# Optimization experiments

Hardware: AMD Instinct MI355X
Metric: run time of the kernel (lower is better)

## Reference

```python
import jax, jax.numpy as jnp
import numpy as np

N = 20000      # nodes
E = 160000     # edges
F_IN = 64      # node_feature_dim
HID = 256      # hidden_dim (= per-head out_channels, concat=False)
HEADS = 4
OUT = 2
BN_EPS = 1e-5


def setup_inputs() -> dict:
    key = jax.random.key(0)
    ks = jax.random.split(key, 24)
    s = 0.02

    def w(k, shape):
        return jax.random.normal(k, shape, jnp.float32) * s

    return {
        "node_feature": jax.random.normal(ks[0], (N, F_IN), jnp.float32),
        "edge_index": jax.random.randint(ks[1], (2, E), 0, N, jnp.int32),
        # layer 1 (in=F_IN)
        "wq1": w(ks[2], (F_IN, HEADS * HID)), "bq1": w(ks[3], (HEADS * HID,)),
        "wk1": w(ks[4], (F_IN, HEADS * HID)), "bk1": w(ks[5], (HEADS * HID,)),
        "wv1": w(ks[6], (F_IN, HEADS * HID)), "bv1": w(ks[7], (HEADS * HID,)),
        "ws1": w(ks[8], (F_IN, HID)),        "bs1": w(ks[9], (HID,)),
        # layer 2 (in=HID)
        "wq2": w(ks[10], (HID, HEADS * HID)), "bq2": w(ks[11], (HEADS * HID,)),
        "wk2": w(ks[12], (HID, HEADS * HID)), "bk2": w(ks[13], (HEADS * HID,)),
        "wv2": w(ks[14], (HID, HEADS * HID)), "bv2": w(ks[15], (HEADS * HID,)),
        "ws2": w(ks[16], (HID, HID)),         "bs2": w(ks[17], (HID,)),
        # batch norm affine
        "bn_gamma": jnp.ones((HID,), jnp.float32) + w(ks[18], (HID,)),
        "bn_beta": w(ks[19], (HID,)),
        # final linear
        "lin_w": w(ks[20], (HID, OUT)), "lin_b": w(ks[21], (OUT,)),
    }


def _transformer_conv(x, src, dst, wq, bq, wk, bk, wv, bv, ws, bs):
    """PyG TransformerConv, heads=HEADS, concat=False (mean over heads), root_weight."""
    n = x.shape[0]
    q = (x @ wq + bq).reshape(n, HEADS, HID)   # [N,H,C]
    k = (x @ wk + bk).reshape(n, HEADS, HID)
    v = (x @ wv + bv).reshape(n, HEADS, HID)
    # per-edge attention logits: q_i . k_j / sqrt(C)   (message j->i, i = dst)
    alpha = jnp.einsum('ehc,ehc->eh', q[dst], k[src]) / jnp.sqrt(jnp.float32(HID))  # [E,H]
    # scatter-softmax over incoming edges of each target node
    m = jax.ops.segment_max(alpha, dst, num_segments=n)
    m = jnp.where(jnp.isfinite(m), m, 0.0)  # nodes with no in-edges
    ex = jnp.exp(alpha - m[dst])
    denom = jax.ops.segment_sum(ex, dst, num_segments=n)
    a = ex / (denom[dst] + 1e-16)                          # [E,H]
    out = jax.ops.segment_sum(v[src] * a[..., None], dst, num_segments=n)  # [N,H,C]
    return out.mean(axis=1) + x @ ws + bs                  # concat=False -> head mean; + skip


def reference(node_feature, edge_index,
              wq1, bq1, wk1, bk1, wv1, bv1, ws1, bs1,
              wq2, bq2, wk2, bk2, wv2, bv2, ws2, bs2,
              bn_gamma, bn_beta, lin_w, lin_b):
    src, dst = edge_index[0], edge_index[1]
    x = _transformer_conv(node_feature, src, dst, wq1, bq1, wk1, bk1, wv1, bv1, ws1, bs1)
    x = _transformer_conv(x, src, dst, wq2, bq2, wk2, bk2, wv2, bv2, ws2, bs2)
    # BatchNorm1d (training mode: batch statistics, biased variance)
    mu = x.mean(axis=0)
    var = jnp.mean(jnp.square(x - mu), axis=0)
    x = bn_gamma * (x - mu) / jnp.sqrt(var + BN_EPS) + bn_beta
    rsu_embedding = x[0:1]                     # [1, HID]
    logits = jax.nn.relu(x @ lin_w + lin_b)    # [N, OUT]
    action_prob = jax.nn.softmax(logits, axis=1)
    return (action_prob, rsu_embedding)
```

## Files before the change

### kernel.cpp

```cpp
#include <hip/hip_runtime.h>
#include <hip/hip_bf16.h>
#include <math.h>

#define DI __device__ __forceinline__

constexpr int NN   = 20000;
constexpr int NE   = 160000;
constexpr int FIN  = 64;
constexpr int HIDC = 256;
constexpr int NH   = 4;
constexpr int NOUT = 3328;
constexpr int CAPD = 128;

typedef __attribute__((ext_vector_type(8))) short short8;
typedef __attribute__((ext_vector_type(4))) float f32x4;
typedef __attribute__((ext_vector_type(2))) float f32x2;

DI float bf2f(unsigned short u) { return __uint_as_float(((unsigned)u) << 16); }

DI void gld16(const void* g, void* l) {
  __builtin_amdgcn_global_load_lds((const __attribute__((address_space(1))) unsigned*)g,
                                   (__attribute__((address_space(3))) unsigned*)l, 16, 0, 0);
}

DI unsigned fp8pack4(float a, float b, float c, float d) {
  int v = __builtin_amdgcn_cvt_pk_fp8_f32(a, b, 0, false);
  v = __builtin_amdgcn_cvt_pk_fp8_f32(c, d, v, true);
  return (unsigned)v;
}

__global__ void k_prep(const float* __restrict__ x, __hip_bfloat16* __restrict__ xb,
                       const int* __restrict__ dst, int* __restrict__ deg) {
  int gid = blockIdx.x * 256 + threadIdx.x;
  if (gid < NN * FIN) xb[gid] = __float2bfloat16(x[gid]);
  if (gid < NE) atomicAdd(&deg[dst[gid]], 1);
}

__global__ void k_scan(const int* __restrict__ deg, int* __restrict__ offs,
                       int* __restrict__ cursor, int n_) {
  __shared__ int part[1024];
  int tid = threadIdx.x;
  const int CH = (n_ + 1023) >> 10;
  int base = tid * CH;
  int s = 0;
  for (int i = 0; i < CH; ++i) { int idx = base + i; if (idx < n_) s += deg[idx]; }
  part[tid] = s;
  __syncthreads();
  for (int off = 1; off < 1024; off <<= 1) {
    int v = (tid >= off) ? part[tid - off] : 0;
    __syncthreads();
    part[tid] += v;
    __syncthreads();
  }
  int run = (tid == 0) ? 0 : part[tid - 1];
  for (int i = 0; i < CH; ++i) {
    int idx = base + i;
    if (idx < n_) { offs[idx] = run; cursor[idx] = run; run += deg[idx]; }
  }
  if (tid == 1023) offs[n_] = run;
}

__global__ void k_scatter(const int* __restrict__ dst, int* __restrict__ cursor,
                          int* __restrict__ eid, int e_) {
  int e = blockIdx.x * blockDim.x + threadIdx.x;
  if (e < e_) {
    int p = atomicAdd(&cursor[dst[e]], 1);
    eid[p] = e;
  }
}

template <int K>
__global__ void k_pack(const float* __restrict__ wq, const float* __restrict__ bq,
                       const float* __restrict__ wk, const float* __restrict__ bk,
                       const float* __restrict__ wv, const float* __restrict__ bv,
                       const float* __restrict__ ws, const float* __restrict__ bs,
                       __hip_bfloat16* __restrict__ Wt, float* __restrict__ biasp) {
  int n = blockIdx.x * 128 + threadIdx.x;
  int k = blockIdx.y;
  const float* w; const float* b; int off; int M;
  if (n < 1024)      { w = wq; b = bq; off = n;        M = 1024; }
  else if (n < 2048) { w = wk; b = bk; off = n - 1024; M = 1024; }
  else if (n < 3072) { w = wv; b = bv; off = n - 2048; M = 1024; }
  else               { w = ws; b = bs; off = n - 3072; M = 256;  }
  Wt[(size_t)n * K + k] = __float2bfloat16(w[(size_t)k * M + off]);
  if (k == 0) biasp[n] = b[off];
}

template <int K>
__global__ __launch_bounds__(64, 2) void k_gemm_pw(
    const __hip_bfloat16* __restrict__ X, const __hip_bfloat16* __restrict__ Wt,
    const float* __restrict__ biasp,
    unsigned char* __restrict__ qb, unsigned char* __restrict__ kb,
    unsigned char* __restrict__ vb, __hip_bfloat16* __restrict__ skipb,
    int nrows, int NCB, int NCH, int TPC, int RT) {
  __shared__ char lds[16384 + 2304];
  const int l = threadIdx.x;

  const int nwg = NCB * NCH;
  const int per = nwg >> 3;
  const int w = (blockIdx.x & 7) * per + (blockIdx.x >> 3);
  const int chunk = w / NCB;
  const int ct = w % NCB;
  const int bn = ct * 64;
  const int t0 = chunk * TPC;
  int t1 = t0 + TPC; if (t1 > RT) t1 = RT;
  constexpr int KT = K / 64;
  constexpr int NS = K / 32;

  const int lm = l & 15, lk = l >> 4;

  short8 bfr[4 * NS];
  {
    const __hip_bfloat16* bp = Wt + (size_t)(bn + lm) * K + lk * 8;
#pragma unroll
    for (int n = 0; n < 4; ++n)
#pragma unroll
      for (int s = 0; s < NS; ++s)
        bfr[n * NS + s] = *(const short8*)(bp + (size_t)n * 16 * K + s * 32);
  }
  float bia[4];
#pragma unroll
  for (int n = 0; n < 4; ++n) bia[n] = biasp[bn + n * 16 + lm];

  unsigned char* dst8 = nullptr; int cb8 = 0;
  if (bn < 1024)      { dst8 = qb; cb8 = bn; }
  else if (bn < 2048) { dst8 = kb; cb8 = bn - 1024; }
  else if (bn < 3072) { dst8 = vb; cb8 = bn - 2048; }

  const int jrow = l >> 3;
  const int cslot = (l & 7) ^ jrow;
  auto STAGE = [&](int buf, int t, int kt) {
    char* db = lds + buf * 8192;
#pragma unroll
    for (int j = 0; j < 8; ++j) {
      int r = t * 64 + j * 8 + jrow;
      if (r >= nrows) r = nrows - 1;
      gld16(X + (size_t)r * K + kt * 64 + cslot * 8, db + j * 1024 + l * 16);
    }
  };

  int buf = 0;
  STAGE(0, t0, 0);
  for (int t = t0; t < t1; ++t) {
    f32x4 acc[4][4] = {};
#pragma unroll
    for (int kt = 0; kt < KT; ++kt) {
      int nt = t, nk = kt + 1;
      if (nk == KT) { nt = (t + 1 < t1) ? t + 1 : t; nk = 0; }
      STAGE(buf ^ 1, nt, nk);
      asm volatile("s_waitcnt vmcnt(8)" ::: "memory");
      const char* db = lds + buf * 8192;
#pragma unroll
      for (int s2 = 0; s2 < 2; ++s2) {
        short8 a[4];
#pragma unroll
        for (int m = 0; m < 4; ++m) {
          int row = m * 16 + lm;
          a[m] = *(const short8*)(db + row * 128 + (((s2 * 4 + lk) ^ (lm & 7)) * 16));
        }
#pragma unroll
        for (int m = 0; m < 4; ++m)
#pragma unroll
          for (int n = 0; n < 4; ++n)
            acc[m][n] = __builtin_amdgcn_mfma_f32_16x16x32_bf16(
                a[m], bfr[n * NS + kt * 2 + s2], acc[m][n], 0, 0, 0);
      }
      buf ^= 1;
    }

    char* sc = lds + 16384;
    const int tbase = t * 64;
    const int srow = l >> 2, qc = l & 3;
#pragma unroll
    for (int m = 0; m < 4; ++m) {
#pragma unroll
      for (int n = 0; n < 4; ++n)
#pragma unroll
        for (int r = 0; r < 4; ++r)
          *(__hip_bfloat16*)(sc + (lk * 4 + r) * 144 + (n * 16 + lm) * 2) =
              __float2bfloat16(acc[m][n][r] + bia[n]);
      const char* sr = sc + srow * 144 + qc * 32;
      short8 ta = *(const short8*)(sr);
      short8 tb = *(const short8*)(sr + 16);
      int grow = tbase + m * 16 + srow;
      if (grow < nrows) {
        if (dst8 != nullptr) {
          uint4 d;
          d.x = fp8pack4(bf2f((unsigned short)ta[0]), bf2f((unsigned short)ta[1]),
                         bf2f((unsigned short)ta[2]), bf2f((unsigned short)ta[3]));
          d.y = fp8pack4(bf2f((unsigned short)ta[4]), bf2f((unsigned short)ta[5]),
                         bf2f((unsigned short)ta[6]), bf2f((unsigned short)ta[7]));
          d.z = fp8pack4(bf2f((unsigned short)tb[0]), bf2f((unsigned short)tb[1]),
                         bf2f((unsigned short)tb[2]), bf2f((unsigned short)tb[3]));
          d.w = fp8pack4(bf2f((unsigned short)tb[4]), bf2f((unsigned short)tb[5]),
                         bf2f((unsigned short)tb[6]), bf2f((unsigned short)tb[7]));
          *(uint4*)(dst8 + (size_t)grow * 1024 + cb8 + qc * 16) = d;
        } else {
          __hip_bfloat16* sp = skipb + (size_t)grow * HIDC + (bn - 3072) + qc * 16;
          *(short8*)(sp) = ta;
          *(short8*)(sp + 8) = tb;
        }
      }
    }
  }
  asm volatile("s_waitcnt vmcnt(0)" ::: "memory");
}

__global__ __launch_bounds__(256) void k_attn(
    const unsigned char* __restrict__ qb, const unsigned char* __restrict__ kb,
    const unsigned char* __restrict__ vb,
    const int* __restrict__ offs, const int* __restrict__ eid,
    const int* __restrict__ src, const __hip_bfloat16* __restrict__ skipb,
    __hip_bfloat16* __restrict__ outb, float* __restrict__ outf) {
  int n = blockIdx.x;
  int s0 = offs[n], s1 = offs[n + 1];
  int deg = s1 - s0;
  int tid = threadIdx.x;
  if (deg == 0) {
    if (tid < 64) {
      int c = tid * 4;
      ushort4 sv = *(const ushort4*)((const ushort*)skipb + (size_t)n * HIDC + c);
      if (outb != nullptr) *(ushort4*)((ushort*)outb + (size_t)n * HIDC + c) = sv;
      if (outf != nullptr) {
        float* xr = outf + (size_t)n * HIDC + c;
        xr[0] = bf2f(sv.x); xr[1] = bf2f(sv.y); xr[2] = bf2f(sv.z); xr[3] = bf2f(sv.w);
      }
    }
    return;
  }
  __shared__ int ses[CAPD];
  __shared__ float red[NH][HIDC];
  int h = tid >> 6, lane = tid & 63;
  int dc = deg < CAPD ? deg : CAPD;
  for (int i = tid; i < dc; i += 256) ses[i] = src[eid[s0 + i]];
  __syncthreads();

  const int hc = h * HIDC;
  int c = lane * 4;
  unsigned qu = *(const unsigned*)(qb + (size_t)n * 1024 + hc + c);
  f32x2 q01 = __builtin_amdgcn_cvt_pk_f32_fp8(qu, false);
  f32x2 q23 = __builtin_amdgcn_cvt_pk_f32_fp8(qu, true);
  float qx = q01.x, qy = q01.y, qz = q23.x, qw = q23.y;

  float denom = 0.f;
  float4 acc = make_float4(0.f, 0.f, 0.f, 0.f);
  int sc0 = ses[0];
  unsigned ku0 = *(const unsigned*)(kb + (size_t)sc0 * 1024 + hc + c);
  unsigned vu0 = *(const unsigned*)(vb + (size_t)sc0 * 1024 + hc + c);
  for (int i = 0; i < deg; ++i) {
    unsigned ku1 = 0, vu1 = 0;
    if (i + 1 < deg) {
      int s1i = (i + 1 < CAPD) ? ses[i + 1] : src[eid[s0 + i + 1]];
      ku1 = *(const unsigned*)(kb + (size_t)s1i * 1024 + hc + c);
      vu1 = *(const unsigned*)(vb + (size_t)s1i * 1024 + hc + c);
    }
    f32x2 k01 = __builtin_amdgcn_cvt_pk_f32_fp8(ku0, false);
    f32x2 k23 = __builtin_amdgcn_cvt_pk_f32_fp8(ku0, true);
    float p = qx * k01.x + qy * k01.y + qz * k23.x + qw * k23.y;
#pragma unroll
    for (int off = 32; off > 0; off >>= 1) p += __shfl_xor(p, off);
    float wgt = __expf(p * 0.0625f);
    denom += wgt;
    f32x2 v01 = __builtin_amdgcn_cvt_pk_f32_fp8(vu0, false);
    f32x2 v23 = __builtin_amdgcn_cvt_pk_f32_fp8(vu0, true);
    acc.x = fmaf(wgt, v01.x, acc.x);
    acc.y = fmaf(wgt, v01.y, acc.y);
    acc.z = fmaf(wgt, v23.x, acc.z);
    acc.w = fmaf(wgt, v23.y, acc.w);
    ku0 = ku1; vu0 = vu1;
  }
  float dinv = 1.f / (denom + 1e-16f);
  red[h][c + 0] = acc.x * dinv;
  red[h][c + 1] = acc.y * dinv;
  red[h][c + 2] = acc.z * dinv;
  red[h][c + 3] = acc.w * dinv;
  __syncthreads();
  if (tid < 64) {
    int c0 = tid * 4;
    ushort4 sv = *(const ushort4*)((const ushort*)skipb + (size_t)n * HIDC + c0);
    float sk[4] = {bf2f(sv.x), bf2f(sv.y), bf2f(sv.z), bf2f(sv.w)};
#pragma unroll
    for (int j = 0; j < 4; ++j) {
      float m = (red[0][c0 + j] + red[1][c0 + j] + red[2][c0 + j] + red[3][c0 + j]) * 0.25f;
      float val = m + sk[j];
      if (outb != nullptr) ((ushort*)outb)[(size_t)n * HIDC + c0 + j] = (ushort)(__bfloat16_as_ushort(__float2bfloat16(val)));
      if (outf != nullptr) outf[(size_t)n * HIDC + c0 + j] = val;
    }
  }
}

__global__ void k_bnstats(const float* __restrict__ x, float* __restrict__ sums,
                          float* __restrict__ sumsq, int n_) {
  int t = threadIdx.x;
  float s = 0.f, s2 = 0.f;
  for (int r = blockIdx.x; r < n_; r += gridDim.x) {
    float vv = x[(size_t)r * HIDC + t];
    s += vv; s2 += vv * vv;
  }
  atomicAdd(&sums[t], s);
  atomicAdd(&sumsq[t], s2);
}

__global__ __launch_bounds__(256) void k_final(
    const float* __restrict__ x, const float* __restrict__ sums, const float* __restrict__ sumsq,
    const float* __restrict__ gamma, const float* __restrict__ beta,
    const float* __restrict__ lw, const float* __restrict__ lb,
    float* __restrict__ out, int n_) {
  int sub = threadIdx.x >> 6, lane = threadIdx.x & 63;
  int n = blockIdx.x * 4 + sub;
  if (n >= n_) return;
  int c = lane * 4;
  float4 sm  = *(const float4*)(sums + c);
  float4 sq  = *(const float4*)(sumsq + c);
  const float inv_n = 1.f / (float)n_;
  float mu0 = sm.x * inv_n, mu1 = sm.y * inv_n, mu2 = sm.z * inv_n, mu3 = sm.w * inv_n;
  float r0 = 1.f / sqrtf(fmaxf(sq.x * inv_n - mu0 * mu0, 0.f) + 1e-5f);
  float r1 = 1.f / sqrtf(fmaxf(sq.y * inv_n - mu1 * mu1, 0.f) + 1e-5f);
  float r2 = 1.f / sqrtf(fmaxf(sq.z * inv_n - mu2 * mu2, 0.f) + 1e-5f);
  float r3 = 1.f / sqrtf(fmaxf(sq.w * inv_n - mu3 * mu3, 0.f) + 1e-5f);
  const float* xr = x + (size_t)n * HIDC;
  float4 xv = *(const float4*)(xr + c);
  float4 gv = *(const float4*)(gamma + c);
  float4 bv = *(const float4*)(beta + c);
  float y0 = gv.x * (xv.x - mu0) * r0 + bv.x;
  float y1 = gv.y * (xv.y - mu1) * r1 + bv.y;
  float y2 = gv.z * (xv.z - mu2) * r2 + bv.z;
  float y3 = gv.w * (xv.w - mu3) * r3 + bv.w;
  float4 wa = *(const float4*)(lw + (size_t)c * 2);
  float4 wb = *(const float4*)(lw + (size_t)c * 2 + 4);
  float p0 = y0 * wa.x + y1 * wa.z + y2 * wb.x + y3 * wb.z;
  float p1 = y0 * wa.y + y1 * wa.w + y2 * wb.y + y3 * wb.w;
#pragma unroll
  for (int off = 32; off > 0; off >>= 1) {
    p0 += __shfl_xor(p0, off);
    p1 += __shfl_xor(p1, off);
  }
  if (n == 0) *(float4*)(out + (size_t)NN * 2 + c) = make_float4(y0, y1, y2, y3);
  if (lane == 0) {
    float l0 = fmaxf(p0 + lb[0], 0.f);
    float l1 = fmaxf(p1 + lb[1], 0.f);
    float m = fmaxf(l0, l1);
    float e0 = expf(l0 - m), e1 = expf(l1 - m);
    float inv = 1.f / (e0 + e1);
    out[(size_t)n * 2 + 0] = e0 * inv;
    out[(size_t)n * 2 + 1] = e1 * inv;
  }
}

extern "C" void kernel_launch(void* const* d_in, const int* in_sizes, int n_in,
                              void* d_out, int out_size, void* d_ws, size_t ws_size,
                              hipStream_t stream) {
  const float* x0  = (const float*)d_in[0];
  const int*   ei  = (const int*)d_in[1];
  const float* wq1 = (const float*)d_in[2];  const float* bq1 = (const float*)d_in[3];
  const float* wk1 = (const float*)d_in[4];  const float* bk1 = (const float*)d_in[5];
  const float* wv1 = (const float*)d_in[6];  const float* bv1 = (const float*)d_in[7];
  const float* ws1 = (const float*)d_in[8];  const float* bs1 = (const float*)d_in[9];
  const float* wq2 = (const float*)d_in[10]; const float* bq2 = (const float*)d_in[11];
  const float* wk2 = (const float*)d_in[12]; const float* bk2 = (const float*)d_in[13];
  const float* wv2 = (const float*)d_in[14]; const float* bv2 = (const float*)d_in[15];
  const float* ws2 = (const float*)d_in[16]; const float* bs2 = (const float*)d_in[17];
  const float* gam = (const float*)d_in[18]; const float* bet = (const float*)d_in[19];
  const float* lw  = (const float*)d_in[20]; const float* lb  = (const float*)d_in[21];
  const int* srcv = ei;
  const int* dstv = ei + NE;

  char* p = (char*)d_ws;
  auto take = [&](size_t bytes) {
    char* r = p;
    p += (bytes + 255) & ~(size_t)255;
    return r;
  };
  unsigned char* qbuf = (unsigned char*)take((size_t)NN * 1024);
  unsigned char* kbuf = (unsigned char*)take((size_t)NN * 1024);
  unsigned char* vbuf = (unsigned char*)take((size_t)NN * 1024);
  __hip_bfloat16* skipb = (__hip_bfloat16*)take((size_t)NN * HIDC * 2);
  __hip_bfloat16* x0b = (__hip_bfloat16*)take((size_t)NN * FIN * 2);
  __hip_bfloat16* x2b = (__hip_bfloat16*)take((size_t)NN * HIDC * 2);
  __hip_bfloat16* Wt  = (__hip_bfloat16*)take((size_t)NOUT * HIDC * 2);
  float* x3    = (float*)take((size_t)NN * HIDC * 4);
  float* biasp = (float*)take((size_t)NOUT * 4);
  float* bnbuf = (float*)take(2 * HIDC * 4);
  int* deg    = (int*)take((size_t)NN * 4);
  int* offs   = (int*)take((size_t)(NN + 1) * 4);
  int* cursor = (int*)take((size_t)NN * 4);
  int* eidb   = (int*)take((size_t)NE * 4);
  if ((size_t)(p - (char*)d_ws) > ws_size) return;

  float* sums  = bnbuf;
  float* sumsq = bnbuf + HIDC;

  hipMemsetAsync(deg, 0, (size_t)NN * 4, stream);
  hipMemsetAsync(bnbuf, 0, 2 * HIDC * 4, stream);
  k_prep<<<(NN * FIN + 255) / 256, 256, 0, stream>>>(x0, x0b, dstv, deg);
  k_scan<<<1, 1024, 0, stream>>>(deg, offs, cursor, NN);
  k_scatter<<<(NE + 255) / 256, 256, 0, stream>>>(dstv, cursor, eidb, NE);

  const int RT  = (NN + 63) / 64;
  const int NCB = NOUT / 64;
  const int NCH = 40;
  const int TPC = (RT + NCH - 1) / NCH;
  const int GRID = NCB * NCH;
  k_pack<FIN><<<dim3(NOUT / 128, FIN), 128, 0, stream>>>(wq1, bq1, wk1, bk1, wv1, bv1, ws1, bs1, Wt, biasp);
  k_gemm_pw<FIN><<<GRID, 64, 0, stream>>>(x0b, Wt, biasp, qbuf, kbuf, vbuf, skipb, NN, NCB, NCH, TPC, RT);
  k_attn<<<NN, 256, 0, stream>>>(qbuf, kbuf, vbuf, offs, eidb, srcv, skipb, x2b, nullptr);
  k_pack<HIDC><<<dim3(NOUT / 128, HIDC), 128, 0, stream>>>(wq2, bq2, wk2, bk2, wv2, bv2, ws2, bs2, Wt, biasp);
  k_gemm_pw<HIDC><<<GRID, 64, 0, stream>>>(x2b, Wt, biasp, qbuf, kbuf, vbuf, skipb, NN, NCB, NCH, TPC, RT);
  k_attn<<<NN, 256, 0, stream>>>(qbuf, kbuf, vbuf, offs, eidb, srcv, skipb, nullptr, x3);
  k_bnstats<<<256, 256, 0, stream>>>(x3, sums, sumsq, NN);
  k_final<<<(NN + 3) / 4, 256, 0, stream>>>(x3, sums, sumsq, gam, bet, lw, lb, (float*)d_out, NN);
}
```

Before: 362.8 us.

## Store Q/K/V in bf16 and skip in fp32, restructure edge-parallel attention

Q/K/V intermediates move from fp8 to bf16 and the skip branch from bf16 to fp32. That doubles Q/K/V memory traffic but improves accuracy. The attention kernel now processes four edges at once per head, with each lane handling 16 channels and partial sums reduced by shuffles. The in-edge lists are sorted per node so results are deterministic. BatchNorm statistics use a two-stage reduction instead of float atomics, which makes the sums order-independent. Overall this mainly trades bandwidth for precision and determinism, and it adds a sort kernel and an extra reduction launch.

```diff
diff --git a/kernel.cpp b/kernel.cpp
--- a/kernel.cpp
+++ b/kernel.cpp
@@ -14,19 +14,12 @@
 
 typedef __attribute__((ext_vector_type(8))) short short8;
 typedef __attribute__((ext_vector_type(4))) float f32x4;
-typedef __attribute__((ext_vector_type(2))) float f32x2;
 
 DI float bf2f(unsigned short u) { return __uint_as_float(((unsigned)u) << 16); }
 
 DI void gld16(const void* g, void* l) {
   __builtin_amdgcn_global_load_lds((const __attribute__((address_space(1))) unsigned*)g,
                                    (__attribute__((address_space(3))) unsigned*)l, 16, 0, 0);
-}
-
-DI unsigned fp8pack4(float a, float b, float c, float d) {
-  int v = __builtin_amdgcn_cvt_pk_fp8_f32(a, b, 0, false);
-  v = __builtin_amdgcn_cvt_pk_fp8_f32(c, d, v, true);
-  return (unsigned)v;
 }
 
 __global__ void k_prep(const float* __restrict__ x, __hip_bfloat16* __restrict__ xb,
@@ -69,6 +62,18 @@
   }
 }
 
+__global__ void k_sort(const int* __restrict__ offs, int* __restrict__ eid, int n_) {
+  int n = blockIdx.x * 256 + threadIdx.x;
+  if (n >= n_) return;
+  int s0 = offs[n], s1 = offs[n + 1];
+  for (int i = s0 + 1; i < s1; ++i) {
+    int v = eid[i];
+    int j = i - 1;
+    while (j >= s0 && eid[j] > v) { eid[j + 1] = eid[j]; --j; }
+    eid[j + 1] = v;
+  }
+}
+
 template <int K>
 __global__ void k_pack(const float* __restrict__ wq, const float* __restrict__ bq,
                        const float* __restrict__ wk, const float* __restrict__ bk,
@@ -90,8 +95,8 @@
 __global__ __launch_bounds__(64, 2) void k_gemm_pw(
     const __hip_bfloat16* __restrict__ X, const __hip_bfloat16* __restrict__ Wt,
     const float* __restrict__ biasp,
-    unsigned char* __restrict__ qb, unsigned char* __restrict__ kb,
-    unsigned char* __restrict__ vb, __hip_bfloat16* __restrict__ skipb,
+    __hip_bfloat16* __restrict__ qb, __hip_bfloat16* __restrict__ kb,
+    __hip_bfloat16* __restrict__ vb, float* __restrict__ skipf,
     int nrows, int NCB, int NCH, int TPC, int RT) {
   __shared__ char lds[16384 + 2304];
   const int l = threadIdx.x;
@@ -122,10 +127,10 @@
 #pragma unroll
   for (int n = 0; n < 4; ++n) bia[n] = biasp[bn + n * 16 + lm];
 
-  unsigned char* dst8 = nullptr; int cb8 = 0;
-  if (bn < 1024)      { dst8 = qb; cb8 = bn; }
-  else if (bn < 2048) { dst8 = kb; cb8 = bn - 1024; }
-  else if (bn < 3072) { dst8 = vb; cb8 = bn - 2048; }
+  __hip_bfloat16* dst16 = nullptr; int cb16 = 0;
+  if (bn < 1024)      { dst16 = qb; cb16 = bn; }
+  else if (bn < 2048) { dst16 = kb; cb16 = bn - 1024; }
+  else if (bn < 3072) { dst16 = vb; cb16 = bn - 2048; }
 
   const int jrow = l >> 3;
   const int cslot = (l & 7) ^ jrow;
@@ -168,49 +173,49 @@
       buf ^= 1;
     }
 
-    char* sc = lds + 16384;
     const int tbase = t * 64;
-    const int srow = l >> 2, qc = l & 3;
-#pragma unroll
-    for (int m = 0; m < 4; ++m) {
-#pragma unroll
-      for (int n = 0; n < 4; ++n)
-#pragma unroll
-        for (int r = 0; r < 4; ++r)
-          *(__hip_bfloat16*)(sc + (lk * 4 + r) * 144 + (n * 16 + lm) * 2) =
-              __float2bfloat16(acc[m][n][r] + bia[n]);
-      const char* sr = sc + srow * 144 + qc * 32;
-      short8 ta = *(const short8*)(sr);
-      short8 tb = *(const short8*)(sr + 16);
-      int grow = tbase + m * 16 + srow;
-      if (grow < nrows) {
-        if (dst8 != nullptr) {
-          uint4 d;
-          d.x = fp8pack4(bf2f((unsigned short)ta[0]), bf2f((unsigned short)ta[1]),
-                         bf2f((unsigned short)ta[2]), bf2f((unsigned short)ta[3]));
-          d.y = fp8pack4(bf2f((unsigned short)ta[4]), bf2f((unsigned short)ta[5]),
-                         bf2f((unsigned short)ta[6]), bf2f((unsigned short)ta[7]));
-          d.z = fp8pack4(bf2f((unsigned short)tb[0]), bf2f((unsigned short)tb[1]),
-                         bf2f((unsigned short)tb[2]), bf2f((unsigned short)tb[3]));
-          d.w = fp8pack4(bf2f((unsigned short)tb[4]), bf2f((unsigned short)tb[5]),
-                         bf2f((unsigned short)tb[6]), bf2f((unsigned short)tb[7]));
-          *(uint4*)(dst8 + (size_t)grow * 1024 + cb8 + qc * 16) = d;
-        } else {
-          __hip_bfloat16* sp = skipb + (size_t)grow * HIDC + (bn - 3072) + qc * 16;
-          *(short8*)(sp) = ta;
-          *(short8*)(sp + 8) = tb;
+    if (dst16 != nullptr) {
+      char* sc = lds + 16384;
+      const int srow = l >> 2, qc = l & 3;
+#pragma unroll
+      for (int m = 0; m < 4; ++m) {
+#pragma unroll
+        for (int n = 0; n < 4; ++n)
+#pragma unroll
+          for (int r = 0; r < 4; ++r)
+            *(__hip_bfloat16*)(sc + (lk * 4 + r) * 144 + (n * 16 + lm) * 2) =
+                __float2bfloat16(acc[m][n][r] + bia[n]);
+        const char* sr = sc + srow * 144 + qc * 32;
+        short8 ta = *(const short8*)(sr);
+        short8 tb = *(const short8*)(sr + 16);
+        int grow = tbase + m * 16 + srow;
+        if (grow < nrows) {
+          ushort* o = (ushort*)dst16 + (size_t)grow * 1024 + cb16 + qc * 16;
+          *(short8*)o = ta;
+          *(short8*)(o + 8) = tb;
         }
       }
+    } else {
+      const int cb = bn - 3072;
+#pragma unroll
+      for (int m = 0; m < 4; ++m)
+#pragma unroll
+        for (int n = 0; n < 4; ++n)
+#pragma unroll
+          for (int r = 0; r < 4; ++r) {
+            int row = tbase + m * 16 + lk * 4 + r;
+            if (row < nrows) skipf[(size_t)row * HIDC + cb + n * 16 + lm] = acc[m][n][r] + bia[n];
+          }
     }
   }
   asm volatile("s_waitcnt vmcnt(0)" ::: "memory");
 }
 
 __global__ __launch_bounds__(256) void k_attn(
-    const unsigned char* __restrict__ qb, const unsigned char* __restrict__ kb,
-    const unsigned char* __restrict__ vb,
+    const __hip_bfloat16* __restrict__ qb, const __hip_bfloat16* __restrict__ kb,
+    const __hip_bfloat16* __restrict__ vb,
     const int* __restrict__ offs, const int* __restrict__ eid,
-    const int* __restrict__ src, const __hip_bfloat16* __restrict__ skipb,
+    const int* __restrict__ src, const float* __restrict__ skipf,
     __hip_bfloat16* __restrict__ outb, float* __restrict__ outf) {
   int n = blockIdx.x;
   int s0 = offs[n], s1 = offs[n + 1];
@@ -219,86 +224,117 @@
   if (deg == 0) {
     if (tid < 64) {
       int c = tid * 4;
-      ushort4 sv = *(const ushort4*)((const ushort*)skipb + (size_t)n * HIDC + c);
-      if (outb != nullptr) *(ushort4*)((ushort*)outb + (size_t)n * HIDC + c) = sv;
-      if (outf != nullptr) {
-        float* xr = outf + (size_t)n * HIDC + c;
-        xr[0] = bf2f(sv.x); xr[1] = bf2f(sv.y); xr[2] = bf2f(sv.z); xr[3] = bf2f(sv.w);
+      float4 sv = *(const float4*)(skipf + (size_t)n * HIDC + c);
+      if (outb != nullptr) {
+        ushort* ob = (ushort*)outb + (size_t)n * HIDC + c;
+        ob[0] = __bfloat16_as_ushort(__float2bfloat16(sv.x));
+        ob[1] = __bfloat16_as_ushort(__float2bfloat16(sv.y));
+        ob[2] = __bfloat16_as_ushort(__float2bfloat16(sv.z));
+        ob[3] = __bfloat16_as_ushort(__float2bfloat16(sv.w));
       }
+      if (outf != nullptr) *(float4*)(outf + (size_t)n * HIDC + c) = sv;
     }
     return;
   }
   __shared__ int ses[CAPD];
   __shared__ float red[NH][HIDC];
   int h = tid >> 6, lane = tid & 63;
+  int g = lane >> 4, j = lane & 15;
   int dc = deg < CAPD ? deg : CAPD;
   for (int i = tid; i < dc; i += 256) ses[i] = src[eid[s0 + i]];
   __syncthreads();
 
-  const int hc = h * HIDC;
-  int c = lane * 4;
-  unsigned qu = *(const unsigned*)(qb + (size_t)n * 1024 + hc + c);
-  f32x2 q01 = __builtin_amdgcn_cvt_pk_f32_fp8(qu, false);
-  f32x2 q23 = __builtin_amdgcn_cvt_pk_f32_fp8(qu, true);
-  float qx = q01.x, qy = q01.y, qz = q23.x, qw = q23.y;
-
+  float q[16];
+  {
+    const ushort* qr = (const ushort*)qb + (size_t)n * 1024 + h * 256 + j * 16;
+    short8 q0 = *(const short8*)(qr);
+    short8 q1 = *(const short8*)(qr + 8);
+#pragma unroll
+    for (int d = 0; d < 8; ++d) { q[d] = bf2f((unsigned short)q0[d]); q[8 + d] = bf2f((unsigned short)q1[d]); }
+  }
+
+  float acc[16];
+#pragma unroll
+  for (int d = 0; d < 16; ++d) acc[d] = 0.f;
   float denom = 0.f;
-  float4 acc = make_float4(0.f, 0.f, 0.f, 0.f);
-  int sc0 = ses[0];
-  unsigned ku0 = *(const unsigned*)(kb + (size_t)sc0 * 1024 + hc + c);
-  unsigned vu0 = *(const unsigned*)(vb + (size_t)sc0 * 1024 + hc + c);
-  for (int i = 0; i < deg; ++i) {
-    unsigned ku1 = 0, vu1 = 0;
-    if (i + 1 < deg) {
-      int s1i = (i + 1 < CAPD) ? ses[i + 1] : src[eid[s0 + i + 1]];
-      ku1 = *(const unsigned*)(kb + (size_t)s1i * 1024 + hc + c);
-      vu1 = *(const unsigned*)(vb + (size_t)s1i * 1024 + hc + c);
-    }
-    f32x2 k01 = __builtin_amdgcn_cvt_pk_f32_fp8(ku0, false);
-    f32x2 k23 = __builtin_amdgcn_cvt_pk_f32_fp8(ku0, true);
-    float p = qx * k01.x + qy * k01.y + qz * k23.x + qw * k23.y;
-#pragma unroll
-    for (int off = 32; off > 0; off >>= 1) p += __shfl_xor(p, off);
-    float wgt = __expf(p * 0.0625f);
+
+  for (int i0 = 0; i0 < deg; i0 += 4) {
+    int e = i0 + g;
+    bool valid = e < deg;
+    int s;
+    if (valid) s = (e < CAPD) ? ses[e] : src[eid[s0 + e]];
+    else       s = ses[0];
+    const ushort* kr = (const ushort*)kb + (size_t)s * 1024 + h * 256 + j * 16;
+    short8 k0 = *(const short8*)(kr);
+    short8 k1 = *(const short8*)(kr + 8);
+    const ushort* vr = (const ushort*)vb + (size_t)s * 1024 + h * 256 + j * 16;
+    short8 v0 = *(const short8*)(vr);
+    short8 v1 = *(const short8*)(vr + 8);
+    float p = 0.f;
+#pragma unroll
+    for (int d = 0; d < 8; ++d) {
+      p = fmaf(q[d], bf2f((unsigned short)k0[d]), p);
+      p = fmaf(q[8 + d], bf2f((unsigned short)k1[d]), p);
+    }
+    p += __shfl_xor(p, 1);
+    p += __shfl_xor(p, 2);
+    p += __shfl_xor(p, 4);
+    p += __shfl_xor(p, 8);
+    float wgt = valid ? __expf(p * 0.0625f) : 0.f;
     denom += wgt;
-    f32x2 v01 = __builtin_amdgcn_cvt_pk_f32_fp8(vu0, false);
-    f32x2 v23 = __builtin_amdgcn_cvt_pk_f32_fp8(vu0, true);
-    acc.x = fmaf(wgt, v01.x, acc.x);
-    acc.y = fmaf(wgt, v01.y, acc.y);
-    acc.z = fmaf(wgt, v23.x, acc.z);
-    acc.w = fmaf(wgt, v23.y, acc.w);
-    ku0 = ku1; vu0 = vu1;
-  }
+#pragma unroll
+    for (int d = 0; d < 8; ++d) {
+      acc[d] = fmaf(wgt, bf2f((unsigned short)v0[d]), acc[d]);
+      acc[8 + d] = fmaf(wgt, bf2f((unsigned short)v1[d]), acc[8 + d]);
+    }
+  }
+
+#pragma unroll
+  for (int d = 0; d < 16; ++d) {
+    acc[d] += __shfl_xor(acc[d], 16);
+    acc[d] += __shfl_xor(acc[d], 32);
+  }
+  denom += __shfl_xor(denom, 16);
+  denom += __shfl_xor(denom, 32);
   float dinv = 1.f / (denom + 1e-16f);
-  red[h][c + 0] = acc.x * dinv;
-  red[h][c + 1] = acc.y * dinv;
-  red[h][c + 2] = acc.z * dinv;
-  red[h][c + 3] = acc.w * dinv;
+  if (g == 0) {
+#pragma unroll
+    for (int d = 0; d < 16; ++d) red[h][j * 16 + d] = acc[d] * dinv;
+  }
   __syncthreads();
   if (tid < 64) {
     int c0 = tid * 4;
-    ushort4 sv = *(const ushort4*)((const ushort*)skipb + (size_t)n * HIDC + c0);
-    float sk[4] = {bf2f(sv.x), bf2f(sv.y), bf2f(sv.z), bf2f(sv.w)};
-#pragma unroll
-    for (int j = 0; j < 4; ++j) {
-      float m = (red[0][c0 + j] + red[1][c0 + j] + red[2][c0 + j] + red[3][c0 + j]) * 0.25f;
-      float val = m + sk[j];
-      if (outb != nullptr) ((ushort*)outb)[(size_t)n * HIDC + c0 + j] = (ushort)(__bfloat16_as_ushort(__float2bfloat16(val)));
-      if (outf != nullptr) outf[(size_t)n * HIDC + c0 + j] = val;
-    }
-  }
-}
-
-__global__ void k_bnstats(const float* __restrict__ x, float* __restrict__ sums,
-                          float* __restrict__ sumsq, int n_) {
+    float4 sv = *(const float4*)(skipf + (size_t)n * HIDC + c0);
+    float sk[4] = {sv.x, sv.y, sv.z, sv.w};
+#pragma unroll
+    for (int jj = 0; jj < 4; ++jj) {
+      float m = (red[0][c0 + jj] + red[1][c0 + jj] + red[2][c0 + jj] + red[3][c0 + jj]) * 0.25f;
+      float val = m + sk[jj];
+      if (outb != nullptr) ((ushort*)outb)[(size_t)n * HIDC + c0 + jj] = __bfloat16_as_ushort(__float2bfloat16(val));
+      if (outf != nullptr) outf[(size_t)n * HIDC + c0 + jj] = val;
+    }
+  }
+}
+
+__global__ void k_bnstats(const float* __restrict__ x, float* __restrict__ psum,
+                          float* __restrict__ psumsq) {
+  int t = threadIdx.x, b = blockIdx.x;
+  float s = 0.f, s2 = 0.f;
+  for (int r = b; r < NN; r += 256) {
+    float vv = x[(size_t)r * HIDC + t];
+    s += vv; s2 += vv * vv;
+  }
+  psum[b * HIDC + t] = s;
+  psumsq[b * HIDC + t] = s2;
+}
+
+__global__ void k_bnred(const float* __restrict__ psum, const float* __restrict__ psumsq,
+                        float* __restrict__ sums, float* __restrict__ sumsq) {
   int t = threadIdx.x;
   float s = 0.f, s2 = 0.f;
-  for (int r = blockIdx.x; r < n_; r += gridDim.x) {
-    float vv = x[(size_t)r * HIDC + t];
-    s += vv; s2 += vv * vv;
-  }
-  atomicAdd(&sums[t], s);
-  atomicAdd(&sumsq[t], s2);
+  for (int b = 0; b < 256; ++b) { s += psum[b * HIDC + t]; s2 += psumsq[b * HIDC + t]; }
+  sums[t] = s;
+  sumsq[t] = s2;
 }
 
 __global__ __launch_bounds__(256) void k_final(
@@ -371,15 +407,17 @@
     p += (bytes + 255) & ~(size_t)255;
     return r;
   };
-  unsigned char* qbuf = (unsigned char*)take((size_t)NN * 1024);
-  unsigned char* kbuf = (unsigned char*)take((size_t)NN * 1024);
-  unsigned char* vbuf = (unsigned char*)take((size_t)NN * 1024);
-  __hip_bfloat16* skipb = (__hip_bfloat16*)take((size_t)NN * HIDC * 2);
+  __hip_bfloat16* qbuf = (__hip_bfloat16*)take((size_t)NN * 1024 * 2);
+  __hip_bfloat16* kbuf = (__hip_bfloat16*)take((size_t)NN * 1024 * 2);
+  __hip_bfloat16* vbuf = (__hip_bfloat16*)take((size_t)NN * 1024 * 2);
+  float* skipf = (float*)take((size_t)NN * HIDC * 4);
   __hip_bfloat16* x0b = (__hip_bfloat16*)take((size_t)NN * FIN * 2);
   __hip_bfloat16* x2b = (__hip_bfloat16*)take((size_t)NN * HIDC * 2);
   __hip_bfloat16* Wt  = (__hip_bfloat16*)take((size_t)NOUT * HIDC * 2);
   float* x3    = (float*)take((size_t)NN * HIDC * 4);
   float* biasp = (float*)take((size_t)NOUT * 4);
+  float* psum  = (float*)take(256 * HIDC * 4);
+  float* psumsq= (float*)take(256 * HIDC * 4);
   float* bnbuf = (float*)take(2 * HIDC * 4);
   int* deg    = (int*)take((size_t)NN * 4);
   int* offs   = (int*)take((size_t)(NN + 1) * 4);
@@ -391,10 +429,10 @@
   float* sumsq = bnbuf + HIDC;
 
   hipMemsetAsync(deg, 0, (size_t)NN * 4, stream);
-  hipMemsetAsync(bnbuf, 0, 2 * HIDC * 4, stream);
   k_prep<<<(NN * FIN + 255) / 256, 256, 0, stream>>>(x0, x0b, dstv, deg);
   k_scan<<<1, 1024, 0, stream>>>(deg, offs, cursor, NN);
   k_scatter<<<(NE + 255) / 256, 256, 0, stream>>>(dstv, cursor, eidb, NE);
+  k_sort<<<(NN + 255) / 256, 256, 0, stream>>>(offs, eidb, NN);
 
   const int RT  = (NN + 63) / 64;
   const int NCB = NOUT / 64;
@@ -402,11 +440,12 @@
   const int TPC = (RT + NCH - 1) / NCH;
   const int GRID = NCB * NCH;
   k_pack<FIN><<<dim3(NOUT / 128, FIN), 128, 0, stream>>>(wq1, bq1, wk1, bk1, wv1, bv1, ws1, bs1, Wt, biasp);
-  k_gemm_pw<FIN><<<GRID, 64, 0, stream>>>(x0b, Wt, biasp, qbuf, kbuf, vbuf, skipb, NN, NCB, NCH, TPC, RT);
-  k_attn<<<NN, 256, 0, stream>>>(qbuf, kbuf, vbuf, offs, eidb, srcv, skipb, x2b, nullptr);
+  k_gemm_pw<FIN><<<GRID, 64, 0, stream>>>(x0b, Wt, biasp, qbuf, kbuf, vbuf, skipf, NN, NCB, NCH, TPC, RT);
+  k_attn<<<NN, 256, 0, stream>>>(qbuf, kbuf, vbuf, offs, eidb, srcv, skipf, x2b, nullptr);
   k_pack<HIDC><<<dim3(NOUT / 128, HIDC), 128, 0, stream>>>(wq2, bq2, wk2, bk2, wv2, bv2, ws2, bs2, Wt, biasp);
-  k_gemm_pw<HIDC><<<GRID, 64, 0, stream>>>(x2b, Wt, biasp, qbuf, kbuf, vbuf, skipb, NN, NCB, NCH, TPC, RT);
-  k_attn<<<NN, 256, 0, stream>>>(qbuf, kbuf, vbuf, offs, eidb, srcv, skipb, nullptr, x3);
-  k_bnstats<<<256, 256, 0, stream>>>(x3, sums, sumsq, NN);
+  k_gemm_pw<HIDC><<<GRID, 64, 0, stream>>>(x2b, Wt, biasp, qbuf, kbuf, vbuf, skipf, NN, NCB, NCH, TPC, RT);
+  k_attn<<<NN, 256, 0, stream>>>(qbuf, kbuf, vbuf, offs, eidb, srcv, skipf, nullptr, x3);
+  k_bnstats<<<256, 256, 0, stream>>>(x3, psum, psumsq);
+  k_bnred<<<1, 256, 0, stream>>>(psum, psumsq, sums, sumsq);
   k_final<<<(NN + 3) / 4, 256, 0, stream>>>(x3, sums, sumsq, gam, bet, lw, lb, (float*)d_out, NN);
 }
```

After: 461.1 us. +27.1%, slower.
